# Performance work log

Measured on AMD Instinct MI355X. Metric: run time of the kernel, lower is better.

## Reference

```python
import jax, jax.numpy as jnp
import numpy as np
from math import sqrt

B, S, D_MODEL, H, DK, DV = 16, 512, 256, 8, 32, 32
EPS = 1e-5


def layer_norm(x, g, b):
    m = jnp.mean(x, axis=-1, keepdims=True)
    v = jnp.mean((x - m) ** 2, axis=-1, keepdims=True)
    return g * (x - m) / jnp.sqrt(v + EPS) + b


def setup_inputs() -> dict:
    key = jax.random.key(0)
    ks = jax.random.split(key, 16)
    inp = {
        "input_Q": jax.random.normal(ks[0], (B, S, D_MODEL), jnp.float32),
        "input_K": jax.random.normal(ks[1], (B, S, D_MODEL), jnp.float32),
        "input_V": jax.random.normal(ks[2], (B, S, D_MODEL), jnp.float32),
        "attn_mask": jax.random.bernoulli(ks[3], 0.1, (B, H, S, S)),
        "matrix": jax.random.uniform(ks[4], (B, S, S), jnp.float32),
        # learned params (stored [in, out], i.e. transpose of torch Linear weight)
        "W_Q": jax.random.normal(ks[5], (D_MODEL, H * DK), jnp.float32) * 0.02,
        "W_K": jax.random.normal(ks[6], (D_MODEL, H * DK), jnp.float32) * 0.02,
        "W_V": jax.random.normal(ks[7], (D_MODEL, H * DV), jnp.float32) * 0.02,
        "W_V2": jax.random.normal(ks[8], (D_MODEL, DV), jnp.float32) * 0.02,
        "W_fc": jax.random.normal(ks[9], (DV * (H + 1), D_MODEL), jnp.float32) * 0.02,
        "ln_g": jnp.ones((D_MODEL,), jnp.float32),
        "ln_b": jnp.zeros((D_MODEL,), jnp.float32),
        "fu_ln_g": jnp.ones((H + 1,), jnp.float32),
        "fu_ln_b": jnp.zeros((H + 1,), jnp.float32),
        "fu_w1": jax.random.normal(ks[10], (H + 1, 6), jnp.float32) * 0.3,
        "fu_b1": jnp.zeros((6,), jnp.float32),
        "fu_w2": jax.random.normal(ks[11], (6, 1), jnp.float32) * 0.3,
        "fu_b2": jnp.zeros((1,), jnp.float32),
    }
    return inp


def reference(input_Q, input_K, input_V, attn_mask, matrix,
              W_Q, W_K, W_V, W_V2, W_fc, ln_g, ln_b,
              fu_ln_g, fu_ln_b, fu_w1, fu_b1, fu_w2, fu_b2):
    b = input_Q.shape[0]
    # project and split heads: [B, H, S, d]
    Q = (input_Q @ W_Q).reshape(b, -1, H, DK).transpose(0, 2, 1, 3)
    K = (input_K @ W_K).reshape(b, -1, H, DK).transpose(0, 2, 1, 3)
    V = (input_V @ W_V).reshape(b, -1, H, DV).transpose(0, 2, 1, 3)
    scores = jnp.einsum('bhqd,bhkd->bhqk', Q, K) / sqrt(DK)
    scores = jnp.where(attn_mask, -1e9, scores)
    attn = jax.nn.softmax(scores, axis=-1)            # [B, H, S, S]
    context = jnp.einsum('bhqk,bhkd->bhqd', attn, V)  # [B, H, S, DV]
    # second context from pairwise matrix
    context2 = matrix @ (input_V @ W_V2)              # [B, S, DV]
    # gated matrix update: concat matrix with attn maps along head axis
    gate_in = jnp.concatenate([matrix[:, None], attn], axis=1)  # [B, H+1, S, S]
    gate_in = gate_in.transpose(0, 3, 2, 1)                     # [B, S, S, H+1]
    g = layer_norm(gate_in, fu_ln_g, fu_ln_b)
    g = jax.nn.relu(g @ fu_w1 + fu_b1)
    g = jax.nn.sigmoid(g @ fu_w2 + fu_b2)[..., 0]               # [B, S, S]
    matrix_out = matrix * g
    # merge heads, concat, project, layernorm
    context = context.transpose(0, 2, 1, 3).reshape(b, -1, H * DV)
    context = jnp.concatenate([context, context2], axis=-1)     # [B, S, DV*(H+1)]
    output = layer_norm(context @ W_fc, ln_g, ln_b)
    return (output, matrix_out)
```

## Files before the change

### kernel.cpp

```cpp
#include <hip/hip_runtime.h>
#include <hip/hip_bf16.h>

#define BB 16
#define SS 512
#define DM 256
#define NH 8

#define OFF_QB    0
#define OFF_KB    1048576
#define OFF_VT    2097152
#define OFF_VP2   3145728
#define OFF_CTXB  3407872
#define OFF_CTX2B 4456448
#define OFF_G     4587520
#define OFF_FLAG  6684672

#define SCALE 0.17677669529663687f

typedef __attribute__((ext_vector_type(8))) short bfrag8;
typedef __attribute__((ext_vector_type(4))) float facc4;

__global__ void mask_or_kernel(const unsigned int* __restrict__ w,
                               unsigned int* __restrict__ acc) {
  __shared__ unsigned int sh[256];
  unsigned int a = 0;
  int base = blockIdx.x * 1024;
  for (int i = threadIdx.x; i < 1024; i += 256) a |= w[base + i];
  sh[threadIdx.x] = a;
  __syncthreads();
  for (int s = 128; s > 0; s >>= 1) {
    if (threadIdx.x < s) sh[threadIdx.x] |= sh[threadIdx.x + s];
    __syncthreads();
  }
  if (threadIdx.x == 0) atomicOr(acc, sh[0]);
}

__global__ __launch_bounds__(256) void gemm_qkv_kernel(
    const float* __restrict__ inQ, const float* __restrict__ inK,
    const float* __restrict__ inV,
    const float* __restrict__ Wq, const float* __restrict__ Wk,
    const float* __restrict__ Wv,
    __hip_bfloat16* __restrict__ Qb, __hip_bfloat16* __restrict__ Kb,
    __hip_bfloat16* __restrict__ Vt) {
  __shared__ __align__(16) __hip_bfloat16 As[64][40];
  __shared__ __align__(16) __hip_bfloat16 Bs[64][40];
  const int tid = threadIdx.x;
  const int bid = blockIdx.x;
  const int matid = bid >> 9;
  const int mblk = (bid & 511) >> 2;
  const int nblk = bid & 3;
  const int m0 = mblk * 64;
  const int n0 = nblk * 64;
  const float* X = (matid == 0) ? inQ : (matid == 1) ? inK : inV;
  const float* W = (matid == 0) ? Wq : (matid == 1) ? Wk : Wv;

  const int lane = tid & 63;
  const int w = tid >> 6;
  const int wm = w & 1, wn = w >> 1;
  const int cl = lane & 15, quad = lane >> 4;
  const int arow = tid >> 2, ak8 = (tid & 3) * 8;
  const int bn = tid & 63, bk8 = (tid >> 6) * 8;

  facc4 acc[2][2];
#pragma unroll
  for (int t = 0; t < 2; t++)
#pragma unroll
    for (int u = 0; u < 2; u++) acc[t][u] = (facc4){0.f, 0.f, 0.f, 0.f};

#pragma unroll 1
  for (int kc = 0; kc < 8; kc++) {
    float4 x0 = *(const float4*)&X[(m0 + arow) * 256 + kc * 32 + ak8];
    float4 x1 = *(const float4*)&X[(m0 + arow) * 256 + kc * 32 + ak8 + 4];
    float wv[8];
#pragma unroll
    for (int j = 0; j < 8; j++) wv[j] = W[(kc * 32 + bk8 + j) * 256 + n0 + bn];
    __syncthreads();
    {
      __hip_bfloat16 ta[8];
      ta[0] = __float2bfloat16(x0.x); ta[1] = __float2bfloat16(x0.y);
      ta[2] = __float2bfloat16(x0.z); ta[3] = __float2bfloat16(x0.w);
      ta[4] = __float2bfloat16(x1.x); ta[5] = __float2bfloat16(x1.y);
      ta[6] = __float2bfloat16(x1.z); ta[7] = __float2bfloat16(x1.w);
      *(uint4*)&As[arow][ak8] = *(uint4*)ta;
      __hip_bfloat16 tb[8];
#pragma unroll
      for (int j = 0; j < 8; j++) tb[j] = __float2bfloat16(wv[j]);
      *(uint4*)&Bs[bn][bk8] = *(uint4*)tb;
    }
    __syncthreads();
    bfrag8 aA[2], bB[2];
#pragma unroll
    for (int t = 0; t < 2; t++)
      aA[t] = *(const bfrag8*)&As[wm * 32 + t * 16 + cl][quad * 8];
#pragma unroll
    for (int u = 0; u < 2; u++)
      bB[u] = *(const bfrag8*)&Bs[wn * 32 + u * 16 + cl][quad * 8];
#pragma unroll
    for (int t = 0; t < 2; t++)
#pragma unroll
      for (int u = 0; u < 2; u++)
        acc[t][u] =
            __builtin_amdgcn_mfma_f32_16x16x32_bf16(aA[t], bB[u], acc[t][u], 0, 0, 0);
  }

  if (matid < 2) {
    __hip_bfloat16* Y = (matid == 0) ? Qb : Kb;
#pragma unroll
    for (int t = 0; t < 2; t++)
#pragma unroll
      for (int u = 0; u < 2; u++)
#pragma unroll
        for (int reg = 0; reg < 4; reg++)
          Y[(m0 + wm * 32 + t * 16 + quad * 4 + reg) * 256 + n0 + wn * 32 +
            u * 16 + cl] = __float2bfloat16(acc[t][u][reg]);
  } else {
#pragma unroll
    for (int t = 0; t < 2; t++)
#pragma unroll
      for (int u = 0; u < 2; u++) {
        int c = n0 + wn * 32 + u * 16 + cl;
        int mg = m0 + wm * 32 + t * 16 + quad * 4;
        int b = mg >> 9, s = mg & 511;
        __hip_bfloat16 pk[4];
#pragma unroll
        for (int reg = 0; reg < 4; reg++)
          pk[reg] = __float2bfloat16(acc[t][u][reg]);
        *(ushort4*)&Vt[(((b << 8) + c) << 9) + s] = *(ushort4*)pk;
      }
  }
}

__global__ __launch_bounds__(256) void vp2_kernel(
    const float* __restrict__ inV, const float* __restrict__ Wv2,
    float* __restrict__ Vp2) {
  __shared__ __align__(16) float xs[16][260];
  const int t = threadIdx.x;
  const int r0 = blockIdx.x * 16;
  for (int e = t; e < 16 * 256; e += 256) {
    int r = e >> 8, i = e & 255;
    xs[r][i] = inV[(r0 + r) * 256 + i];
  }
  __syncthreads();
  const int c2 = t & 31, rr = t >> 5;
  float a0 = 0.f, a1 = 0.f;
  for (int i = 0; i < 256; i += 4) {
    float w0 = Wv2[i * 32 + c2], w1 = Wv2[(i + 1) * 32 + c2];
    float w2 = Wv2[(i + 2) * 32 + c2], w3 = Wv2[(i + 3) * 32 + c2];
    float4 xa = *(const float4*)&xs[rr][i];
    float4 xb = *(const float4*)&xs[rr + 8][i];
    a0 += xa.x * w0 + xa.y * w1 + xa.z * w2 + xa.w * w3;
    a1 += xb.x * w0 + xb.y * w1 + xb.z * w2 + xb.w * w3;
  }
  Vp2[(r0 + rr) * 32 + c2] = a0;
  Vp2[(r0 + rr + 8) * 32 + c2] = a1;
}

__global__ __launch_bounds__(512) void attn_kernel(
    const __hip_bfloat16* __restrict__ Qb, const __hip_bfloat16* __restrict__ Kb,
    const __hip_bfloat16* __restrict__ Vt, const void* __restrict__ mask,
    const float* __restrict__ matrix,
    const float* __restrict__ fulng, const float* __restrict__ fulnb,
    const float* __restrict__ fuw1, const float* __restrict__ fub1,
    const float* __restrict__ fuw2, const float* __restrict__ fub2,
    __hip_bfloat16* __restrict__ ctxb, __hip_bfloat16* __restrict__ gws,
    const unsigned int* __restrict__ orv) {
  __shared__ __align__(16) __hip_bfloat16 Sb[NH][16][136];
  __shared__ float fup[85];

  const int tid = threadIdx.x;
  const int lane = tid & 63;
  const int h = tid >> 6;
  const int cl = lane & 15, quad = lane >> 4;
  const int b = ((blockIdx.x & 7) << 1) | (blockIdx.x >> 8);
  const int q0 = ((blockIdx.x >> 3) & 31) * 16;

  if (tid < 9) fup[tid] = fulng[tid];
  else if (tid < 18) fup[tid] = fulnb[tid - 9];
  else if (tid < 72) fup[tid] = fuw1[tid - 18];
  else if (tid < 78) fup[tid] = fub1[tid - 72];
  else if (tid < 84) fup[tid] = fuw2[tid - 78];
  else if (tid == 84) fup[tid] = fub2[0];
  const unsigned int rawor = *orv;
  const int flagv = (rawor <= 1u) ? 0 : ((rawor == 0x3F800000u) ? 2 : 1);

  const unsigned char* mask_b = (const unsigned char*)mask;
  const int* mask_i = (const int*)mask;
  const float* mask_f = (const float*)mask;
  const int mbase = ((b * 8 + h) * 512 + q0) * 512;

  const bfrag8 aQ =
      *(const bfrag8*)&Qb[(((b << 9) + q0 + cl) << 8) + h * 32 + quad * 8];
  const __hip_bfloat16* KbB = &Kb[((b << 9) << 8) + h * 32 + quad * 8];
  const __hip_bfloat16* VtB = &Vt[(((b << 8) + h * 32) << 9)];

  float mx[4] = {-3e38f, -3e38f, -3e38f, -3e38f};
#pragma unroll 4
  for (int nt = 0; nt < 32; nt++) {
    bfrag8 bK = *(const bfrag8*)&KbB[(nt * 16 + cl) << 8];
    facc4 cc = {0.f, 0.f, 0.f, 0.f};
    cc = __builtin_amdgcn_mfma_f32_16x16x32_bf16(aQ, bK, cc, 0, 0, 0);
#pragma unroll
    for (int r = 0; r < 4; r++) mx[r] = fmaxf(mx[r], cc[r]);
  }
#pragma unroll
  for (int r = 0; r < 4; r++)
#pragma unroll
    for (int off = 1; off <= 8; off <<= 1)
      mx[r] = fmaxf(mx[r], __shfl_xor(mx[r], off));

  float l[4] = {0.f, 0.f, 0.f, 0.f};
#pragma unroll 2
  for (int nt = 0; nt < 32; nt++) {
    bfrag8 bK = *(const bfrag8*)&KbB[(nt * 16 + cl) << 8];
    facc4 cc = {0.f, 0.f, 0.f, 0.f};
    cc = __builtin_amdgcn_mfma_f32_16x16x32_bf16(aQ, bK, cc, 0, 0, 0);
#pragma unroll
    for (int r = 0; r < 4; r++) {
      int midx = mbase + (quad * 4 + r) * 512 + nt * 16 + cl;
      bool m;
      if (flagv == 1) m = (mask_b[midx] != 0);
      else if (flagv == 0) m = (mask_i[midx] != 0);
      else m = (mask_f[midx] != 0.f);
      float e = m ? 0.f : __expf(SCALE * (cc[r] - mx[r]));
      l[r] += e;
    }
  }
#pragma unroll
  for (int r = 0; r < 4; r++)
#pragma unroll
    for (int off = 1; off <= 8; off <<= 1) l[r] += __shfl_xor(l[r], off);
  float invl[4];
#pragma unroll
  for (int r = 0; r < 4; r++) invl[r] = 1.f / l[r];

  facc4 a0 = {0.f, 0.f, 0.f, 0.f}, a1 = {0.f, 0.f, 0.f, 0.f};
#pragma unroll 1
  for (int c = 0; c < 4; c++) {
    if (c) __syncthreads();
#pragma unroll 2
    for (int nt = c * 8; nt < c * 8 + 8; nt++) {
      bfrag8 bK = *(const bfrag8*)&KbB[(nt * 16 + cl) << 8];
      facc4 cc = {0.f, 0.f, 0.f, 0.f};
      cc = __builtin_amdgcn_mfma_f32_16x16x32_bf16(aQ, bK, cc, 0, 0, 0);
#pragma unroll
      for (int r = 0; r < 4; r++) {
        int midx = mbase + (quad * 4 + r) * 512 + nt * 16 + cl;
        bool m;
        if (flagv == 1) m = (mask_b[midx] != 0);
        else if (flagv == 0) m = (mask_i[midx] != 0);
        else m = (mask_f[midx] != 0.f);
        float e = m ? 0.f : __expf(SCALE * (cc[r] - mx[r]));
        Sb[h][quad * 4 + r][nt * 16 + cl - c * 128] =
            __float2bfloat16(e * invl[r]);
      }
    }
    __syncthreads();

    {
      const int gq = tid >> 5;
      const int k4 = (tid & 31) * 4;
      float4 mrow =
          *(const float4*)&matrix[((b << 9) + q0 + gq) * 512 + c * 128 + k4];
      float p[NH][4];
#pragma unroll
      for (int hh = 0; hh < NH; hh++) {
        ushort4 sv = *(const ushort4*)&Sb[hh][gq][k4];
        p[hh][0] = __bfloat162float(*(__hip_bfloat16*)&sv.x);
        p[hh][1] = __bfloat162float(*(__hip_bfloat16*)&sv.y);
        p[hh][2] = __bfloat162float(*(__hip_bfloat16*)&sv.z);
        p[hh][3] = __bfloat162float(*(__hip_bfloat16*)&sv.w);
      }
      const float mcomp[4] = {mrow.x, mrow.y, mrow.z, mrow.w};
      __hip_bfloat16 gout[4];
#pragma unroll
      for (int i = 0; i < 4; i++) {
        float v[9];
        v[0] = mcomp[i];
#pragma unroll
        for (int t = 0; t < NH; t++) v[1 + t] = p[t][i];
        float mu = 0.f;
#pragma unroll
        for (int t = 0; t < 9; t++) mu += v[t];
        mu *= (1.f / 9.f);
        float var = 0.f;
#pragma unroll
        for (int t = 0; t < 9; t++) {
          float d = v[t] - mu;
          var += d * d;
        }
        var *= (1.f / 9.f);
        float inv = rsqrtf(var + 1e-5f);
        float y[9];
#pragma unroll
        for (int t = 0; t < 9; t++)
          y[t] = fup[t] * (v[t] - mu) * inv + fup[9 + t];
        float o = fup[84];
#pragma unroll
        for (int j = 0; j < 6; j++) {
          float z = fup[72 + j];
#pragma unroll
          for (int t = 0; t < 9; t++) z += y[t] * fup[18 + t * 6 + j];
          z = fmaxf(z, 0.f);
          o += z * fup[78 + j];
        }
        gout[i] = __float2bfloat16(1.f / (1.f + __expf(-o)));
      }
      *(ushort4*)&gws[((b << 9) + q0 + gq) * 512 + c * 128 + k4] =
          *(ushort4*)gout;
    }

#pragma unroll
    for (int ks = 0; ks < 4; ks++) {
      bfrag8 aP = *(const bfrag8*)&Sb[h][cl][ks * 32 + quad * 8];
      bfrag8 b0 =
          *(const bfrag8*)&VtB[(cl << 9) + c * 128 + ks * 32 + quad * 8];
      bfrag8 b1 =
          *(const bfrag8*)&VtB[((16 + cl) << 9) + c * 128 + ks * 32 + quad * 8];
      a0 = __builtin_amdgcn_mfma_f32_16x16x32_bf16(aP, b0, a0, 0, 0, 0);
      a1 = __builtin_amdgcn_mfma_f32_16x16x32_bf16(aP, b1, a1, 0, 0, 0);
    }
  }

#pragma unroll
  for (int r = 0; r < 4; r++) {
    int row = quad * 4 + r;
    ctxb[((b << 9) + q0 + row) * 256 + h * 32 + cl] = __float2bfloat16(a0[r]);
    ctxb[((b << 9) + q0 + row) * 256 + h * 32 + 16 + cl] =
        __float2bfloat16(a1[r]);
  }
}

__global__ __launch_bounds__(256) void mout_kernel(
    const float* __restrict__ matrix, const __hip_bfloat16* __restrict__ g,
    float* __restrict__ mout) {
  __shared__ float Gs[64][65];
  const int tid = threadIdx.x;
  const int b = blockIdx.x >> 6;
  const int j0 = ((blockIdx.x >> 3) & 7) * 64;
  const int i0 = (blockIdx.x & 7) * 64;

  {
    int r = tid >> 2, c0 = (tid & 3) * 16;
    const __hip_bfloat16* gp = g + (((b << 9) + i0 + r) << 9) + j0 + c0;
    ushort us[16];
    *(uint4*)(us) = *(const uint4*)(gp);
    *(uint4*)(us + 8) = *(const uint4*)(gp + 8);
#pragma unroll
    for (int k = 0; k < 16; k++) {
      __hip_bfloat16 hv = *(__hip_bfloat16*)&us[k];
      Gs[r][c0 + k] = __bfloat162float(hv);
    }
  }
  __syncthreads();

  {
    int jj = tid >> 2, ic = (tid & 3) * 16;
    const float* mp = matrix + (((b << 9) + j0 + jj) << 9) + i0 + ic;
    float* op = mout + (((b << 9) + j0 + jj) << 9) + i0 + ic;
#pragma unroll
    for (int v4 = 0; v4 < 4; v4++) {
      float4 m = *(const float4*)(mp + v4 * 4);
      float4 o;
      o.x = m.x * Gs[ic + v4 * 4 + 0][jj];
      o.y = m.y * Gs[ic + v4 * 4 + 1][jj];
      o.z = m.z * Gs[ic + v4 * 4 + 2][jj];
      o.w = m.w * Gs[ic + v4 * 4 + 3][jj];
      *(float4*)(op + v4 * 4) = o;
    }
  }
}

__global__ __launch_bounds__(256) void ctx2_kernel(
    const float* __restrict__ matrix, const float* __restrict__ Vp2,
    __hip_bfloat16* __restrict__ ctx2b) {
  __shared__ __align__(16) float Ms[16][128];
  __shared__ __align__(16) float Vs2t[32][132];
  const int t = threadIdx.x;
  const int b = blockIdx.x >> 5;
  const int s0 = (blockIdx.x & 31) * 16;
  const int dv = t & 31, rg = t >> 5;
  float acc0 = 0.f, acc1 = 0.f;
  for (int kc = 0; kc < 4; kc++) {
    __syncthreads();
#pragma unroll
    for (int it = 0; it < 8; it++) {
      int idx = t + it * 256;
      int r = idx >> 7, cc = idx & 127;
      Ms[r][cc] = matrix[((b << 9) + s0 + r) * 512 + kc * 128 + cc];
    }
#pragma unroll
    for (int it = 0; it < 16; it++) {
      int e = t + it * 256;
      int k = e >> 5, dv2 = e & 31;
      Vs2t[dv2][k] = Vp2[((b << 9) + kc * 128 + k) * 32 + dv2];
    }
    __syncthreads();
    for (int k = 0; k < 128; k += 4) {
      float4 vv = *(const float4*)&Vs2t[dv][k];
      float4 m0 = *(const float4*)&Ms[rg][k];
      float4 m1 = *(const float4*)&Ms[rg + 8][k];
      acc0 += m0.x * vv.x + m0.y * vv.y + m0.z * vv.z + m0.w * vv.w;
      acc1 += m1.x * vv.x + m1.y * vv.y + m1.z * vv.z + m1.w * vv.w;
    }
  }
  ctx2b[((b << 9) + s0 + rg) * 32 + dv] = __float2bfloat16(acc0);
  ctx2b[((b << 9) + s0 + rg + 8) * 32 + dv] = __float2bfloat16(acc1);
}

__global__ __launch_bounds__(256) void final_kernel(
    const __hip_bfloat16* __restrict__ ctxb,
    const __hip_bfloat16* __restrict__ ctx2b, const float* __restrict__ Wfc,
    const float* __restrict__ lng, const float* __restrict__ lnb,
    float* __restrict__ out) {
  __shared__ __align__(16) __hip_bfloat16 As[32][40];
  __shared__ __align__(16) __hip_bfloat16 Bs[256][40];
  __shared__ __align__(16) float xs[32][260];
  __shared__ float red2[32][8][2];
  __shared__ float musig[32][2];
  const int tid = threadIdx.x;
  const int m0 = blockIdx.x * 32;
  const int lane = tid & 63, w = tid >> 6;
  const int cl = lane & 15, quad = lane >> 4;
  const int arow = tid >> 3, ak4 = (tid & 7) * 4;

  facc4 acc[2][4];
#pragma unroll
  for (int t = 0; t < 2; t++)
#pragma unroll
    for (int u = 0; u < 4; u++) acc[t][u] = (facc4){0.f, 0.f, 0.f, 0.f};

#pragma unroll 1
  for (int kc = 0; kc < 9; kc++) {
    ushort4 av;
    if (kc < 8)
      av = *(const ushort4*)&ctxb[(m0 + arow) * 256 + kc * 32 + ak4];
    else
      av = *(const ushort4*)&ctx2b[(m0 + arow) * 32 + ak4];
    float wv[32];
#pragma unroll
    for (int j = 0; j < 32; j++) wv[j] = Wfc[(kc * 32 + j) * 256 + tid];
    __syncthreads();
    *(ushort4*)&As[arow][ak4] = av;
    {
      __hip_bfloat16 tw[32];
#pragma unroll
      for (int j = 0; j < 32; j++) tw[j] = __float2bfloat16(wv[j]);
#pragma unroll
      for (int g = 0; g < 4; g++) *(uint4*)&Bs[tid][g * 8] = *(uint4*)&tw[g * 8];
    }
    __syncthreads();
    bfrag8 aA[2], bB[4];
#pragma unroll
    for (int t = 0; t < 2; t++)
      aA[t] = *(const bfrag8*)&As[t * 16 + cl][quad * 8];
#pragma unroll
    for (int u = 0; u < 4; u++)
      bB[u] = *(const bfrag8*)&Bs[w * 64 + u * 16 + cl][quad * 8];
#pragma unroll
    for (int t = 0; t < 2; t++)
#pragma unroll
      for (int u = 0; u < 4; u++)
        acc[t][u] =
            __builtin_amdgcn_mfma_f32_16x16x32_bf16(aA[t], bB[u], acc[t][u], 0, 0, 0);
  }

#pragma unroll
  for (int t = 0; t < 2; t++)
#pragma unroll
    for (int u = 0; u < 4; u++)
#pragma unroll
      for (int reg = 0; reg < 4; reg++)
        xs[t * 16 + quad * 4 + reg][w * 64 + u * 16 + cl] = acc[t][u][reg];
  __syncthreads();

  {
    int r = tid >> 3, c0 = (tid & 7) * 32;
    float s1 = 0.f, s2 = 0.f;
    for (int j = 0; j < 32; j += 4) {
      float4 v = *(const float4*)&xs[r][c0 + j];
      s1 += v.x + v.y + v.z + v.w;
      s2 += v.x * v.x + v.y * v.y + v.z * v.z + v.w * v.w;
    }
    red2[r][tid & 7][0] = s1;
    red2[r][tid & 7][1] = s2;
  }
  __syncthreads();
  if (tid < 32) {
    float s1 = 0.f, s2 = 0.f;
#pragma unroll
    for (int j = 0; j < 8; j++) {
      s1 += red2[tid][j][0];
      s2 += red2[tid][j][1];
    }
    float mu = s1 * (1.f / 256.f);
    float var = s2 * (1.f / 256.f) - mu * mu;
    musig[tid][0] = mu;
    musig[tid][1] = rsqrtf(var + 1e-5f);
  }
  __syncthreads();
  {
    float gt = lng[tid], bt = lnb[tid];
#pragma unroll 4
    for (int r = 0; r < 32; r++)
      out[(m0 + r) * 256 + tid] =
          gt * (xs[r][tid] - musig[r][0]) * musig[r][1] + bt;
  }
}

extern "C" void kernel_launch(void* const* d_in, const int* in_sizes, int n_in,
                              void* d_out, int out_size, void* d_ws,
                              size_t ws_size, hipStream_t stream) {
  const float* inQ = (const float*)d_in[0];
  const float* inK = (const float*)d_in[1];
  const float* inV = (const float*)d_in[2];
  const void* mask = d_in[3];
  const float* matrix = (const float*)d_in[4];
  const float* Wq = (const float*)d_in[5];
  const float* Wk = (const float*)d_in[6];
  const float* Wv = (const float*)d_in[7];
  const float* Wv2 = (const float*)d_in[8];
  const float* Wfc = (const float*)d_in[9];
  const float* lng = (const float*)d_in[10];
  const float* lnb = (const float*)d_in[11];
  const float* fulng = (const float*)d_in[12];
  const float* fulnb = (const float*)d_in[13];
  const float* fuw1 = (const float*)d_in[14];
  const float* fub1 = (const float*)d_in[15];
  const float* fuw2 = (const float*)d_in[16];
  const float* fub2 = (const float*)d_in[17];

  float* ws = (float*)d_ws;
  __hip_bfloat16* Qb = (__hip_bfloat16*)(ws + OFF_QB);
  __hip_bfloat16* Kb = (__hip_bfloat16*)(ws + OFF_KB);
  __hip_bfloat16* Vt = (__hip_bfloat16*)(ws + OFF_VT);
  float* Vp2 = ws + OFF_VP2;
  __hip_bfloat16* ctxb = (__hip_bfloat16*)(ws + OFF_CTXB);
  __hip_bfloat16* ctx2b = (__hip_bfloat16*)(ws + OFF_CTX2B);
  __hip_bfloat16* gws = (__hip_bfloat16*)(ws + OFF_G);
  unsigned int* flag = (unsigned int*)(ws + OFF_FLAG);

  float* out = (float*)d_out;
  float* mout = out + BB * SS * DM;

  hipMemsetAsync(flag, 0, 4, stream);
  mask_or_kernel<<<64, 256, 0, stream>>>((const unsigned int*)mask, flag);
  gemm_qkv_kernel<<<1536, 256, 0, stream>>>(inQ, inK, inV, Wq, Wk, Wv, Qb, Kb,
                                            Vt);
  vp2_kernel<<<512, 256, 0, stream>>>(inV, Wv2, Vp2);
  attn_kernel<<<512, 512, 0, stream>>>(Qb, Kb, Vt, mask, matrix, fulng, fulnb,
                                       fuw1, fub1, fuw2, fub2, ctxb, gws, flag);
  mout_kernel<<<BB * 64, 256, 0, stream>>>(matrix, gws, mout);
  ctx2_kernel<<<512, 256, 0, stream>>>(matrix, Vp2, ctx2b);
  final_kernel<<<256, 256, 0, stream>>>(ctxb, ctx2b, Wfc, lng, lnb, out);
}
```

Before: 463.1 us.

## Pre-pack attention mask into bitmasks and consume bits in attention kernel

Adds a kernel that reads the attention mask once and packs it into 64-bit ballot words in workspace. The attention kernel then loads one packed word per row for each 64-column chunk and tests bits, instead of doing per-element byte, int or float mask loads with a dtype branch in both the row-sum pass and the probability-write pass. This cuts mask memory traffic and load instruction count inside the attention kernel. The cost is one extra kernel launch, a full mask read inside it, and extra workspace past the flag slot, which must fit in the allocated buffer.

New measurement: 410.9 us. 1.13x faster.

```diff
diff --git a/kernel.cpp b/kernel.cpp
--- a/kernel.cpp
+++ b/kernel.cpp
@@ -14,6 +14,7 @@
 #define OFF_CTX2B 4456448
 #define OFF_G     4587520
 #define OFF_FLAG  6684672
+#define OFF_PM    6684674
 
 #define SCALE 0.17677669529663687f
 
@@ -33,6 +34,31 @@
     __syncthreads();
   }
   if (threadIdx.x == 0) atomicOr(acc, sh[0]);
+}
+
+__global__ __launch_bounds__(256) void mask_pack_kernel(
+    const void* __restrict__ mask, unsigned long long* __restrict__ pm,
+    const unsigned int* __restrict__ orv) {
+  const unsigned int rawor = *orv;
+  const int flagv = (rawor <= 1u) ? 0 : ((rawor == 0x3F800000u) ? 2 : 1);
+  const int lane = threadIdx.x & 63;
+  const int wv = threadIdx.x >> 6;
+  const int w0 = (blockIdx.x * 4 + wv) * 32;
+  const unsigned char* mb = (const unsigned char*)mask;
+  const int* mi = (const int*)mask;
+  const float* mf = (const float*)mask;
+  unsigned long long myw = 0;
+#pragma unroll 4
+  for (int i = 0; i < 32; i++) {
+    long long idx = (long long)(w0 + i) * 64 + lane;
+    bool m;
+    if (flagv == 1) m = (mb[idx] != 0);
+    else if (flagv == 0) m = (mi[idx] != 0);
+    else m = (mf[idx] != 0.f);
+    unsigned long long bits = __ballot(m);
+    if (lane == i) myw = bits;
+  }
+  if (lane < 32) pm[w0 + lane] = myw;
 }
 
 __global__ __launch_bounds__(256) void gemm_qkv_kernel(
@@ -157,13 +183,13 @@
 
 __global__ __launch_bounds__(512) void attn_kernel(
     const __hip_bfloat16* __restrict__ Qb, const __hip_bfloat16* __restrict__ Kb,
-    const __hip_bfloat16* __restrict__ Vt, const void* __restrict__ mask,
+    const __hip_bfloat16* __restrict__ Vt,
+    const unsigned long long* __restrict__ pm,
     const float* __restrict__ matrix,
     const float* __restrict__ fulng, const float* __restrict__ fulnb,
     const float* __restrict__ fuw1, const float* __restrict__ fub1,
     const float* __restrict__ fuw2, const float* __restrict__ fub2,
-    __hip_bfloat16* __restrict__ ctxb, __hip_bfloat16* __restrict__ gws,
-    const unsigned int* __restrict__ orv) {
+    __hip_bfloat16* __restrict__ ctxb, __hip_bfloat16* __restrict__ gws) {
   __shared__ __align__(16) __hip_bfloat16 Sb[NH][16][136];
   __shared__ float fup[85];
 
@@ -180,13 +206,8 @@
   else if (tid < 78) fup[tid] = fub1[tid - 72];
   else if (tid < 84) fup[tid] = fuw2[tid - 78];
   else if (tid == 84) fup[tid] = fub2[0];
-  const unsigned int rawor = *orv;
-  const int flagv = (rawor <= 1u) ? 0 : ((rawor == 0x3F800000u) ? 2 : 1);
-
-  const unsigned char* mask_b = (const unsigned char*)mask;
-  const int* mask_i = (const int*)mask;
-  const float* mask_f = (const float*)mask;
-  const int mbase = ((b * 8 + h) * 512 + q0) * 512;
+
+  const unsigned long long* pmb = pm + (((b * NH + h) << 9) + q0) * 8;
 
   const bfrag8 aQ =
       *(const bfrag8*)&Qb[(((b << 9) + q0 + cl) << 8) + h * 32 + quad * 8];
@@ -210,19 +231,24 @@
 
   float l[4] = {0.f, 0.f, 0.f, 0.f};
 #pragma unroll 2
-  for (int nt = 0; nt < 32; nt++) {
-    bfrag8 bK = *(const bfrag8*)&KbB[(nt * 16 + cl) << 8];
-    facc4 cc = {0.f, 0.f, 0.f, 0.f};
-    cc = __builtin_amdgcn_mfma_f32_16x16x32_bf16(aQ, bK, cc, 0, 0, 0);
-#pragma unroll
-    for (int r = 0; r < 4; r++) {
-      int midx = mbase + (quad * 4 + r) * 512 + nt * 16 + cl;
-      bool m;
-      if (flagv == 1) m = (mask_b[midx] != 0);
-      else if (flagv == 0) m = (mask_i[midx] != 0);
-      else m = (mask_f[midx] != 0.f);
-      float e = m ? 0.f : __expf(SCALE * (cc[r] - mx[r]));
-      l[r] += e;
+  for (int w8 = 0; w8 < 8; w8++) {
+    unsigned long long mw[4];
+#pragma unroll
+    for (int r = 0; r < 4; r++)
+      mw[r] = pmb[(quad * 4 + r) * 8 + w8] >> cl;
+#pragma unroll
+    for (int n4 = 0; n4 < 4; n4++) {
+      const int nt = w8 * 4 + n4;
+      bfrag8 bK = *(const bfrag8*)&KbB[(nt * 16 + cl) << 8];
+      facc4 cc = {0.f, 0.f, 0.f, 0.f};
+      cc = __builtin_amdgcn_mfma_f32_16x16x32_bf16(aQ, bK, cc, 0, 0, 0);
+#pragma unroll
+      for (int r = 0; r < 4; r++) {
+        float e = ((mw[r] >> (n4 * 16)) & 1ULL)
+                      ? 0.f
+                      : __expf(SCALE * (cc[r] - mx[r]));
+        l[r] += e;
+      }
     }
   }
 #pragma unroll
@@ -237,21 +263,26 @@
 #pragma unroll 1
   for (int c = 0; c < 4; c++) {
     if (c) __syncthreads();
-#pragma unroll 2
-    for (int nt = c * 8; nt < c * 8 + 8; nt++) {
-      bfrag8 bK = *(const bfrag8*)&KbB[(nt * 16 + cl) << 8];
-      facc4 cc = {0.f, 0.f, 0.f, 0.f};
-      cc = __builtin_amdgcn_mfma_f32_16x16x32_bf16(aQ, bK, cc, 0, 0, 0);
-#pragma unroll
-      for (int r = 0; r < 4; r++) {
-        int midx = mbase + (quad * 4 + r) * 512 + nt * 16 + cl;
-        bool m;
-        if (flagv == 1) m = (mask_b[midx] != 0);
-        else if (flagv == 0) m = (mask_i[midx] != 0);
-        else m = (mask_f[midx] != 0.f);
-        float e = m ? 0.f : __expf(SCALE * (cc[r] - mx[r]));
-        Sb[h][quad * 4 + r][nt * 16 + cl - c * 128] =
-            __float2bfloat16(e * invl[r]);
+#pragma unroll
+    for (int w8 = c * 2; w8 < c * 2 + 2; w8++) {
+      unsigned long long mw[4];
+#pragma unroll
+      for (int r = 0; r < 4; r++)
+        mw[r] = pmb[(quad * 4 + r) * 8 + w8] >> cl;
+#pragma unroll
+      for (int n4 = 0; n4 < 4; n4++) {
+        const int nt = w8 * 4 + n4;
+        bfrag8 bK = *(const bfrag8*)&KbB[(nt * 16 + cl) << 8];
+        facc4 cc = {0.f, 0.f, 0.f, 0.f};
+        cc = __builtin_amdgcn_mfma_f32_16x16x32_bf16(aQ, bK, cc, 0, 0, 0);
+#pragma unroll
+        for (int r = 0; r < 4; r++) {
+          float e = ((mw[r] >> (n4 * 16)) & 1ULL)
+                        ? 0.f
+                        : __expf(SCALE * (cc[r] - mx[r]));
+          Sb[h][quad * 4 + r][nt * 16 + cl - c * 128] =
+              __float2bfloat16(e * invl[r]);
+        }
       }
     }
     __syncthreads();
@@ -538,17 +569,19 @@
   __hip_bfloat16* ctx2b = (__hip_bfloat16*)(ws + OFF_CTX2B);
   __hip_bfloat16* gws = (__hip_bfloat16*)(ws + OFF_G);
   unsigned int* flag = (unsigned int*)(ws + OFF_FLAG);
+  unsigned long long* pmask = (unsigned long long*)(ws + OFF_PM);
 
   float* out = (float*)d_out;
   float* mout = out + BB * SS * DM;
 
   hipMemsetAsync(flag, 0, 4, stream);
   mask_or_kernel<<<64, 256, 0, stream>>>((const unsigned int*)mask, flag);
+  mask_pack_kernel<<<4096, 256, 0, stream>>>(mask, pmask, flag);
   gemm_qkv_kernel<<<1536, 256, 0, stream>>>(inQ, inK, inV, Wq, Wk, Wv, Qb, Kb,
                                             Vt);
   vp2_kernel<<<512, 256, 0, stream>>>(inV, Wv2, Vp2);
-  attn_kernel<<<512, 512, 0, stream>>>(Qb, Kb, Vt, mask, matrix, fulng, fulnb,
-                                       fuw1, fub1, fuw2, fub2, ctxb, gws, flag);
+  attn_kernel<<<512, 512, 0, stream>>>(Qb, Kb, Vt, pmask, matrix, fulng, fulnb,
+                                       fuw1, fub1, fuw2, fub2, ctxb, gws);
   mout_kernel<<<BB * 64, 256, 0, stream>>>(matrix, gws, mout);
   ctx2_kernel<<<512, 256, 0, stream>>>(matrix, Vp2, ctx2b);
   final_kernel<<<256, 256, 0, stream>>>(ctxb, ctx2b, Wfc, lng, lnb, out);
```
